# Kernel optimization log

Measured on AMD Instinct MI355X. Metric: run time of the kernel, lower is better.

## Reference

```python
import jax, jax.numpy as jnp
import numpy as np

IN_DIM, H, E_DIM = 32, 64, 16
N_NODES, N_EDGES = 50000, 100000


def setup_inputs() -> dict:
    key = jax.random.key(0)
    ks = jax.random.split(key, 12)
    x = jax.random.normal(ks[0], (N_NODES, IN_DIM), dtype=jnp.float32)
    edge_index = jax.random.randint(ks[1], (2, N_EDGES), 0, N_NODES, dtype=jnp.int64)
    edge_attr = jax.random.uniform(ks[2], (N_EDGES, E_DIM), dtype=jnp.float32)
    def lin(k, fan_in, shape):
        return jax.random.normal(k, shape, dtype=jnp.float32) / np.sqrt(fan_in)
    return {
        "x": x,
        "edge_index": edge_index,
        "edge_attr": edge_attr,
        # lin0: Linear(in_dim, h)
        "lin0_w": lin(ks[3], IN_DIM, (H, IN_DIM)),
        "lin0_b": jnp.zeros((H,), jnp.float32),
        # NNConv's edge network: Linear(edge_dim, h*h)
        "nn_w": lin(ks[4], E_DIM, (H * H, E_DIM)),
        "nn_b": jnp.zeros((H * H,), jnp.float32),
        # NNConv root weight [in_ch, out_ch] and bias
        "root": lin(ks[5], H, (H, H)),
        "conv_b": jnp.zeros((H,), jnp.float32),
        # GRU (single layer): weight_ih [3h,h], weight_hh [3h,h], biases [3h]
        "w_ih": lin(ks[6], H, (3 * H, H)),
        "w_hh": lin(ks[7], H, (3 * H, H)),
        "b_ih": jnp.zeros((3 * H,), jnp.float32),
        "b_hh": jnp.zeros((3 * H,), jnp.float32),
    }


def _nnconv(x, src, dst, edge_attr, nn_w, nn_b, root, conv_b, num_nodes):
    # per-edge weight matrices [E, h_in, h_out] from the edge MLP
    W_e = (edge_attr @ nn_w.T + nn_b).reshape(-1, H, H)
    # gather source features, per-edge matvec, scatter-add to destinations
    msg = jnp.einsum('ei,eio->eo', x[src], W_e)          # [E, h]
    agg = jax.ops.segment_sum(msg, dst, num_segments=num_nodes)
    return agg + x @ root + conv_b


def _gru_step(x, h, w_ih, w_hh, b_ih, b_hh):
    gi = x @ w_ih.T + b_ih                                # [N, 3h]
    gh = h @ w_hh.T + b_hh
    i_r, i_z, i_n = jnp.split(gi, 3, axis=-1)
    h_r, h_z, h_n = jnp.split(gh, 3, axis=-1)
    r = jax.nn.sigmoid(i_r + h_r)
    z = jax.nn.sigmoid(i_z + h_z)
    n = jnp.tanh(i_n + r * h_n)
    return (1.0 - z) * n + z * h


def reference(x, edge_index, edge_attr, lin0_w, lin0_b, nn_w, nn_b,
              root, conv_b, w_ih, w_hh, b_ih, b_hh):
    src, dst = edge_index[0], edge_index[1]
    num_nodes = x.shape[0]
    out = jax.nn.relu(x @ lin0_w.T + lin0_b)              # [N, h]
    h = out
    for _ in range(3):
        m = jax.nn.relu(_nnconv(out, src, dst, edge_attr, nn_w, nn_b,
                                root, conv_b, num_nodes))
        h = _gru_step(m, h, w_ih, w_hh, b_ih, b_hh)
        out = h
    return out
```

## Files before the change

### kernel.cpp

```cpp
#include <hip/hip_runtime.h>
#include <hip/hip_bf16.h>

typedef unsigned short u16;
typedef __attribute__((ext_vector_type(8))) _Float16 h8v;
typedef __attribute__((ext_vector_type(4))) float f32x4;

#define CAP 32

static __device__ __forceinline__ u16 f2h(float f) {
    _Float16 h = (_Float16)f;
    u16 r; __builtin_memcpy(&r, &h, 2); return r;
}
static __device__ __forceinline__ float h2f(u16 b) {
    _Float16 h; __builtin_memcpy(&h, &b, 2); return (float)h;
}
static __device__ __forceinline__ float sigm(float x) {
    return 1.f / (1.f + __expf(-x));
}
static __device__ __forceinline__ float tanh_f(float x) {
    return 1.f - 2.f / (__expf(2.f * x) + 1.f);
}

__global__ __launch_bounds__(256) void k_prep(
        const float* __restrict__ nn_w, const float* __restrict__ nn_b,
        const float* __restrict__ root, const float* __restrict__ w_hh,
        const float* __restrict__ w_ih, const float* __restrict__ lin0_w,
        const float* __restrict__ ea,
        u16* __restrict__ wf2, u16* __restrict__ w1, u16* __restrict__ w2,
        u16* __restrict__ w0, u16* __restrict__ ea16, int* __restrict__ deg,
        int N, int nEA) {
    int idx = blockIdx.x * 256 + threadIdx.x;
    if (idx < 34 * 4 * 512) {
        int j = idx & 7, lane = (idx >> 3) & 63;
        int rest = idx >> 9;
        int ct = rest & 3, kc = rest >> 2;
        int kappa = kc * 32 + ((lane >> 4) * 8) + j;
        int o = ct * 16 + (lane & 15);
        float v;
        if (kappa < 1024) {
            int k = kappa >> 6, i = kappa & 63;
            v = nn_w[(size_t)(i * 64 + o) * 16 + k];
        } else {
            v = nn_b[(size_t)(kappa - 1024) * 64 + o];
        }
        wf2[idx] = f2h(v);
    }
    if (idx < 16384 + 12288 + 2048) {
        if (idx < 16384) {
            int j = idx & 7, lane = (idx >> 3) & 63;
            int rest = idx >> 9;
            int ct = rest & 15, kc = rest >> 4;
            int k = kc * 32 + ((lane >> 4) * 8) + j;
            int col = ct * 16 + (lane & 15);
            float v = (col < 64) ? root[(size_t)k * 64 + col]
                                 : w_hh[(size_t)(col - 64) * 64 + k];
            w1[idx] = f2h(v);
        } else if (idx < 16384 + 12288) {
            int i2 = idx - 16384;
            int j = i2 & 7, lane = (i2 >> 3) & 63;
            int rest = i2 >> 9;
            int ct = rest % 12, kc = rest / 12;
            int k = kc * 32 + ((lane >> 4) * 8) + j;
            int col = ct * 16 + (lane & 15);
            w2[i2] = f2h(w_ih[(size_t)col * 64 + k]);
        } else {
            int i3 = idx - 16384 - 12288;
            int j = i3 & 7, lane = (i3 >> 3) & 63;
            int ct = i3 >> 9;
            int k = ((lane >> 4) * 8) + j;
            int col = ct * 16 + (lane & 15);
            w0[i3] = f2h(lin0_w[(size_t)col * 32 + k]);
        }
    }
    if (idx < N) deg[idx] = 0;
    if (idx < nEA) ea16[idx] = f2h(ea[idx]);
}

__global__ __launch_bounds__(256) void k_pre2(
        const int* __restrict__ ei, int* __restrict__ deg, int* __restrict__ tab,
        const float* __restrict__ x_in, const u16* __restrict__ w0,
        const float* __restrict__ lin0_b, float* __restrict__ x0,
        int N, int E) {
    int nbuild = (E + 255) / 256;
    int bid = blockIdx.x;
    int t = threadIdx.x;
    if (bid < nbuild) {
        int e = bid * 256 + t;
        if (e < E) {
            int dst = ei[E + e];
            int pos = atomicAdd(&deg[dst], 1);
            if (pos < CAP) tab[(size_t)dst * CAP + pos] = e;
        }
        return;
    }
    int b2 = bid - nbuild;
    int l = t & 63, w = t >> 6, g = l >> 4;
    int n0 = b2 * 64 + w * 16;
    int node = n0 + (l & 15);
    int nc = node < N ? node : N - 1;
    const float* xrow = x_in + (size_t)nc * 32 + g * 8;
    float4 xa = *(const float4*)(xrow);
    float4 xb = *(const float4*)(xrow + 4);
    h8v xh;
    xh[0] = (_Float16)xa.x; xh[1] = (_Float16)xa.y;
    xh[2] = (_Float16)xa.z; xh[3] = (_Float16)xa.w;
    xh[4] = (_Float16)xb.x; xh[5] = (_Float16)xb.y;
    xh[6] = (_Float16)xb.z; xh[7] = (_Float16)xb.w;
    f32x4 acc[4];
    #pragma unroll
    for (int ct = 0; ct < 4; ct++) {
        h8v wh = *(const h8v*)((const _Float16*)w0 + (ct * 64 + l) * 8);
        acc[ct] = __builtin_amdgcn_mfma_f32_16x16x32_f16(wh, xh, (f32x4)(0.f), 0, 0, 0);
    }
    if (node < N) {
        #pragma unroll
        for (int ct = 0; ct < 4; ct++) {
            int c = ct * 16 + g * 4;
            f32x4 bb = *(const f32x4*)(lin0_b + c);
            f32x4 ov;
            #pragma unroll
            for (int r = 0; r < 4; r++) ov[r] = fmaxf(acc[ct][r] + bb[r], 0.f);
            *(f32x4*)(x0 + (size_t)node * 64 + c) = ov;
        }
    }
}

__global__ __launch_bounds__(256) void k_AB(
        const float* __restrict__ x, const u16* __restrict__ ea16,
        const u16* __restrict__ wf2, const int* __restrict__ ei,
        u16* __restrict__ msg, int E) {
    __shared__ __align__(16) u16 Ab[64 * 512];
    int t = threadIdx.x, l = t & 63, w = t >> 6, g = l >> 4;
    int ctH = blockIdx.y;
    int eblk = blockIdx.x * 256 + w * 64;

    int eact[4];
    h8v xf0[4], xf1[4], eav[4][2];
    #pragma unroll
    for (int et = 0; et < 4; et++) {
        int e = eblk + et * 16 + (l & 15);
        eact[et] = e;
        int ec = e < E ? e : E - 1;
        int src = ei[ec];
        const float* xr = x + (size_t)src * 64 + g * 8;
        float4 v0 = *(const float4*)(xr);
        float4 v1 = *(const float4*)(xr + 4);
        float4 v2 = *(const float4*)(xr + 32);
        float4 v3 = *(const float4*)(xr + 36);
        h8v a, b;
        a[0] = (_Float16)v0.x; a[1] = (_Float16)v0.y;
        a[2] = (_Float16)v0.z; a[3] = (_Float16)v0.w;
        a[4] = (_Float16)v1.x; a[5] = (_Float16)v1.y;
        a[6] = (_Float16)v1.z; a[7] = (_Float16)v1.w;
        b[0] = (_Float16)v2.x; b[1] = (_Float16)v2.y;
        b[2] = (_Float16)v2.z; b[3] = (_Float16)v2.w;
        b[4] = (_Float16)v3.x; b[5] = (_Float16)v3.y;
        b[6] = (_Float16)v3.z; b[7] = (_Float16)v3.w;
        xf0[et] = a;
        xf1[et] = b;
        const _Float16* ep = (const _Float16*)ea16 + (size_t)ec * 16;
        eav[et][0] = *(const h8v*)(ep);
        eav[et][1] = *(const h8v*)(ep + 8);
    }

    const uint4* wf2u = (const uint4*)wf2;
    uint4* Abu = (uint4*)Ab;
    #pragma unroll
    for (int i = 0; i < 16; i++) {
        int j = i * 256 + t;
        int f = j >> 6, win = j & 63;
        int gf = (f >> 1) * 4 + ctH * 2 + (f & 1);
        Abu[j] = wf2u[(size_t)gf * 64 + win];
    }
    __syncthreads();

    f32x4 acc[4][2];
    #pragma unroll
    for (int et = 0; et < 4; et++)
        #pragma unroll
        for (int ct = 0; ct < 2; ct++) acc[et][ct] = (f32x4)(0.f);

    const _Float16* AbH = (const _Float16*)Ab;
    const _Float16* wfh = (const _Float16*)wf2;

    #pragma unroll
    for (int p = 0; p < 8; p++) {
        #pragma unroll
        for (int kcl = 0; kcl < 4; kcl++) {
            int kc = p * 4 + kcl;
            h8v af[2];
            #pragma unroll
            for (int ct = 0; ct < 2; ct++)
                af[ct] = *(const h8v*)(AbH + (size_t)(kc * 2 + ct) * 512 + l * 8);
            const int k = 2 * p + (kcl >> 1);
            #pragma unroll
            for (int et = 0; et < 4; et++) {
                _Float16 s = eav[et][k >> 3][k & 7];
                h8v es = {s, s, s, s, s, s, s, s};
                h8v zf = es * ((kcl & 1) ? xf1[et] : xf0[et]);
                #pragma unroll
                for (int ct = 0; ct < 2; ct++)
                    acc[et][ct] = __builtin_amdgcn_mfma_f32_16x16x32_f16(af[ct], zf, acc[et][ct], 0, 0, 0);
            }
        }
    }
    #pragma unroll
    for (int kcl = 0; kcl < 2; kcl++) {
        int kc = 32 + kcl;
        h8v af[2];
        #pragma unroll
        for (int ct = 0; ct < 2; ct++)
            af[ct] = *(const h8v*)(wfh + (size_t)(kc * 4 + ctH * 2 + ct) * 512 + l * 8);
        #pragma unroll
        for (int et = 0; et < 4; et++) {
            h8v zf = (kcl & 1) ? xf1[et] : xf0[et];
            #pragma unroll
            for (int ct = 0; ct < 2; ct++)
                acc[et][ct] = __builtin_amdgcn_mfma_f32_16x16x32_f16(af[ct], zf, acc[et][ct], 0, 0, 0);
        }
    }

    #pragma unroll
    for (int et = 0; et < 4; et++) {
        int e = eact[et];
        if (e < E) {
            u16* mr = msg + (size_t)e * 64 + g * 4;
            #pragma unroll
            for (int ct = 0; ct < 2; ct++) {
                ushort4 pk;
                pk.x = f2h(acc[et][ct][0]);
                pk.y = f2h(acc[et][ct][1]);
                pk.z = f2h(acc[et][ct][2]);
                pk.w = f2h(acc[et][ct][3]);
                *(ushort4*)(mr + (ctH * 2 + ct) * 16) = pk;
            }
        }
    }
}

__global__ __launch_bounds__(256) void k_C(
        const float* __restrict__ x, const u16* __restrict__ msg,
        const int* __restrict__ deg, const int* __restrict__ tab,
        const u16* __restrict__ w1, const u16* __restrict__ w2,
        const float* __restrict__ conv_b, const float* __restrict__ b_hh,
        const float* __restrict__ b_ih, float* __restrict__ hout, int N) {
    __shared__ float mld[4][16][68];
    int t = threadIdx.x, l = t & 63, w = t >> 6, g = l >> 4;
    int n0 = blockIdx.x * 64 + w * 16;
    int node = n0 + (l & 15);
    int nc = node < N ? node : N - 1;
    const float* xrow = x + (size_t)nc * 64 + g * 8;
    const _Float16* w1h = (const _Float16*)w1;
    const _Float16* w2h = (const _Float16*)w2;

    h8v xh[2];
    #pragma unroll
    for (int kc = 0; kc < 2; kc++) {
        f32x4 a = *(const f32x4*)(xrow + kc * 32);
        f32x4 b = *(const f32x4*)(xrow + kc * 32 + 4);
        #pragma unroll
        for (int j = 0; j < 8; j++) xh[kc][j] = (_Float16)(j < 4 ? a[j] : b[j - 4]);
    }

    f32x4 avs[4];
    #pragma unroll
    for (int ct = 0; ct < 4; ct++) avs[ct] = (f32x4)(0.f);
    if (node < N) {
        int dg = deg[node];
        dg = dg < CAP ? dg : CAP;
        const int* tr = tab + (size_t)node * CAP;
        for (int j = 0; j < dg; j++) {
            int eid = tr[j];
            const u16* mr = msg + (size_t)eid * 64 + g * 4;
            #pragma unroll
            for (int ct = 0; ct < 4; ct++) {
                ushort4 mv = *(const ushort4*)(mr + ct * 16);
                avs[ct][0] += h2f(mv.x);
                avs[ct][1] += h2f(mv.y);
                avs[ct][2] += h2f(mv.z);
                avs[ct][3] += h2f(mv.w);
            }
        }
    }

    f32x4 acc1[16];
    #pragma unroll
    for (int ct = 0; ct < 16; ct++) acc1[ct] = (f32x4)(0.f);
    #pragma unroll
    for (int kc = 0; kc < 2; kc++) {
        #pragma unroll
        for (int ct = 0; ct < 16; ct++) {
            h8v wh = *(const h8v*)(w1h + (size_t)(kc * 16 + ct) * 512 + l * 8);
            acc1[ct] = __builtin_amdgcn_mfma_f32_16x16x32_f16(wh, xh[kc], acc1[ct], 0, 0, 0);
        }
    }

    #pragma unroll
    for (int ct = 0; ct < 4; ct++) {
        int c = ct * 16 + g * 4;
        f32x4 cb = *(const f32x4*)(conv_b + c);
        f32x4 mv;
        #pragma unroll
        for (int r = 0; r < 4; r++) mv[r] = fmaxf(acc1[ct][r] + avs[ct][r] + cb[r], 0.f);
        *(f32x4*)(&mld[w][l & 15][c]) = mv;
    }
    #pragma unroll
    for (int ct = 4; ct < 16; ct++) {
        int c = (ct - 4) * 16 + g * 4;
        f32x4 bh = *(const f32x4*)(b_hh + c);
        #pragma unroll
        for (int r = 0; r < 4; r++) acc1[ct][r] += bh[r];
    }
    __syncthreads();

    h8v mh[2];
    #pragma unroll
    for (int kc = 0; kc < 2; kc++) {
        const float* mr = &mld[w][l & 15][kc * 32 + g * 8];
        f32x4 a = *(const f32x4*)(mr);
        f32x4 b = *(const f32x4*)(mr + 4);
        #pragma unroll
        for (int j = 0; j < 8; j++) mh[kc][j] = (_Float16)(j < 4 ? a[j] : b[j - 4]);
    }

    f32x4 acc2[12];
    #pragma unroll
    for (int ct = 0; ct < 12; ct++) acc2[ct] = (f32x4)(0.f);
    #pragma unroll
    for (int kc = 0; kc < 2; kc++) {
        #pragma unroll
        for (int ct = 0; ct < 12; ct++) {
            h8v wh = *(const h8v*)(w2h + (size_t)(kc * 12 + ct) * 512 + l * 8);
            acc2[ct] = __builtin_amdgcn_mfma_f32_16x16x32_f16(wh, mh[kc], acc2[ct], 0, 0, 0);
        }
    }

    #pragma unroll
    for (int q = 0; q < 4; q++) {
        int c = q * 16 + g * 4;
        f32x4 bir = *(const f32x4*)(b_ih + c);
        f32x4 biz = *(const f32x4*)(b_ih + 64 + c);
        f32x4 bin = *(const f32x4*)(b_ih + 128 + c);
        f32x4 hv = (f32x4)(0.f);
        if (node < N) hv = *(const f32x4*)(x + (size_t)node * 64 + c);
        f32x4 outv;
        #pragma unroll
        for (int r = 0; r < 4; r++) {
            float rr = sigm(acc2[q][r] + bir[r] + acc1[4 + q][r]);
            float zz = sigm(acc2[4 + q][r] + biz[r] + acc1[8 + q][r]);
            float nt = tanh_f(acc2[8 + q][r] + bin[r] + rr * acc1[12 + q][r]);
            outv[r] = (1.f - zz) * nt + zz * hv[r];
        }
        if (node < N) *(f32x4*)(hout + (size_t)node * 64 + c) = outv;
    }
}

extern "C" void kernel_launch(void* const* d_in, const int* in_sizes, int n_in,
                              void* d_out, int out_size, void* d_ws, size_t ws_size,
                              hipStream_t stream) {
    const float* x_in   = (const float*)d_in[0];
    const int*   ei     = (const int*)d_in[1];
    const float* ea     = (const float*)d_in[2];
    const float* lin0_w = (const float*)d_in[3];
    const float* lin0_b = (const float*)d_in[4];
    const float* nn_w   = (const float*)d_in[5];
    const float* nn_b   = (const float*)d_in[6];
    const float* root   = (const float*)d_in[7];
    const float* conv_b = (const float*)d_in[8];
    const float* w_ih   = (const float*)d_in[9];
    const float* w_hh   = (const float*)d_in[10];
    const float* b_ih   = (const float*)d_in[11];
    const float* b_hh   = (const float*)d_in[12];

    int N = in_sizes[0] / 32;
    int E = in_sizes[1] / 2;

    char* ws = (char*)d_ws;
    size_t off = 0;
    auto alloc = [&](size_t bytes) { char* p = ws + off; off += (bytes + 255) & ~(size_t)255; return p; };
    float* xbuf   = (float*)alloc((size_t)N * 64 * 4);
    u16*   msg    = (u16*)alloc((size_t)E * 64 * 2);
    u16*   wf2    = (u16*)alloc((size_t)34 * 4 * 512 * 2);
    u16*   ea16   = (u16*)alloc((size_t)E * 16 * 2);
    u16*   w1     = (u16*)alloc(16384 * 2);
    u16*   w2     = (u16*)alloc(12288 * 2);
    u16*   w0     = (u16*)alloc(2048 * 2);
    int*   deg    = (int*)alloc((size_t)N * 4);
    int*   tab    = (int*)alloc((size_t)N * CAP * 4);
    (void)ws_size;

    int nEA = E * 16;
    int nbuild = (E + 255) / 256;
    int ntile  = (N + 63) / 64;

    hipLaunchKernelGGL(k_prep, dim3((nEA + 255) / 256), dim3(256), 0, stream,
                       nn_w, nn_b, root, w_hh, w_ih, lin0_w, ea,
                       wf2, w1, w2, w0, ea16, deg, N, nEA);
    hipLaunchKernelGGL(k_pre2, dim3(nbuild + ntile), dim3(256), 0, stream,
                       ei, deg, tab, x_in, w0, lin0_b, xbuf, N, E);

    for (int it = 0; it < 3; it++) {
        hipLaunchKernelGGL(k_AB, dim3((E + 255) / 256, 2), dim3(256), 0, stream,
                           xbuf, ea16, wf2, ei, msg, E);
        float* hout = (it == 2) ? (float*)d_out : xbuf;
        hipLaunchKernelGGL(k_C, dim3(ntile), dim3(256), 0, stream, xbuf, msg,
                           deg, tab, w1, w2, conv_b, b_hh, b_ih, hout, N);
    }
}
```

Before: 173.6 us.

## Balance per-block edge aggregation via prefix-summed edge list and LDS atomics

Replaces the per-node serial loop over incoming messages with a block-level scheme: wave 0 prefix-sums node degrees, builds a flattened edge list in shared memory, and all 256 threads then gather 16-byte message chunks and accumulate them into a shared aggregation tile with atomicAdd. The aim is to remove load imbalance across degree-varying nodes and widen the memory accesses. In exchange it adds extra __syncthreads barriers, LDS atomic traffic, and about 17KB more shared memory per block, which may lower occupancy.

```diff
diff --git a/kernel.cpp b/kernel.cpp
--- a/kernel.cpp
+++ b/kernel.cpp
@@ -2,10 +2,12 @@
 #include <hip/hip_bf16.h>
 
 typedef unsigned short u16;
+typedef __attribute__((ext_vector_type(8))) unsigned short us8;
 typedef __attribute__((ext_vector_type(8))) _Float16 h8v;
 typedef __attribute__((ext_vector_type(4))) float f32x4;
 
 #define CAP 32
+#define ECAP 256
 
 static __device__ __forceinline__ u16 f2h(float f) {
     _Float16 h = (_Float16)f;
@@ -245,9 +247,14 @@
         const float* __restrict__ conv_b, const float* __restrict__ b_hh,
         const float* __restrict__ b_ih, float* __restrict__ hout, int N) {
     __shared__ float mld[4][16][68];
+    __shared__ float aggs[64][68];
+    __shared__ int els[ECAP];
+    __shared__ short nds[ECAP];
+    __shared__ int offs[65];
     int t = threadIdx.x, l = t & 63, w = t >> 6, g = l >> 4;
-    int n0 = blockIdx.x * 64 + w * 16;
-    int node = n0 + (l & 15);
+    int n0 = blockIdx.x * 64;
+    int nb = w * 16 + (l & 15);
+    int node = n0 + nb;
     int nc = node < N ? node : N - 1;
     const float* xrow = x + (size_t)nc * 64 + g * 8;
     const _Float16* w1h = (const _Float16*)w1;
@@ -262,26 +269,56 @@
         for (int j = 0; j < 8; j++) xh[kc][j] = (_Float16)(j < 4 ? a[j] : b[j - 4]);
     }
 
+    if (w == 0) {
+        int nd = n0 + l;
+        int d = 0;
+        if (nd < N) { d = deg[nd]; if (d > CAP) d = CAP; }
+        int s = d;
+        #pragma unroll
+        for (int o = 1; o < 64; o <<= 1) {
+            int v = __shfl_up(s, o, 64);
+            if (l >= o) s += v;
+        }
+        offs[l + 1] = s;
+        if (l == 0) offs[0] = 0;
+    }
+    {
+        float* af = &aggs[0][0];
+        for (int i = t; i < 64 * 68; i += 256) af[i] = 0.f;
+    }
+    __syncthreads();
+    int T_e = offs[64];
+
+    for (int base = 0; base < T_e; base += ECAP) {
+        int cnt = T_e - base; if (cnt > ECAP) cnt = ECAP;
+        if (w == 0) {
+            int nd = n0 + l;
+            int d = 0;
+            if (nd < N) { d = deg[nd]; if (d > CAP) d = CAP; }
+            int o = offs[l];
+            const int* tr = tab + (size_t)(nd < N ? nd : 0) * CAP;
+            for (int j = 0; j < d; j++) {
+                int s = o + j - base;
+                if (s >= 0 && s < ECAP) { els[s] = tr[j]; nds[s] = (short)l; }
+            }
+        }
+        __syncthreads();
+        for (int task = t; task < cnt * 8; task += 256) {
+            int s = task >> 3, cq = task & 7;
+            int eid = els[s];
+            int n = nds[s];
+            us8 v = *(const us8*)(msg + (size_t)eid * 64 + cq * 8);
+            #pragma unroll
+            for (int i = 0; i < 8; i++)
+                atomicAdd(&aggs[n][cq * 8 + i], h2f(v[i]));
+        }
+        __syncthreads();
+    }
+
     f32x4 avs[4];
     #pragma unroll
-    for (int ct = 0; ct < 4; ct++) avs[ct] = (f32x4)(0.f);
-    if (node < N) {
-        int dg = deg[node];
-        dg = dg < CAP ? dg : CAP;
-        const int* tr = tab + (size_t)node * CAP;
-        for (int j = 0; j < dg; j++) {
-            int eid = tr[j];
-            const u16* mr = msg + (size_t)eid * 64 + g * 4;
-            #pragma unroll
-            for (int ct = 0; ct < 4; ct++) {
-                ushort4 mv = *(const ushort4*)(mr + ct * 16);
-                avs[ct][0] += h2f(mv.x);
-                avs[ct][1] += h2f(mv.y);
-                avs[ct][2] += h2f(mv.z);
-                avs[ct][3] += h2f(mv.w);
-            }
-        }
-    }
+    for (int ct = 0; ct < 4; ct++)
+        avs[ct] = *(const f32x4*)(&aggs[nb][ct * 16 + g * 4]);
 
     f32x4 acc1[16];
     #pragma unroll
```

Result: slower. 276.3 us (+59.1%).

## Split k_C output columns across wave pairs, each wave covering two node tiles

Applied to the files above, without the earlier changes.

Previously each wave in k_C handled one 16-node tile and computed all 64 output columns, loading the full weight set per wave. Now pairs of waves share two node tiles: each wave computes half of the output column tiles for both node tiles. Each loaded weight fragment therefore feeds two MFMAs, which halves weight loads per wave and the per-wave accumulator count. The trade-off is that each wave now gathers edge messages for two nodes, each over half the channels, so per-lane gather loop iterations double while the bytes loaded per edge halve.

```diff
diff --git a/kernel.cpp b/kernel.cpp
--- a/kernel.cpp
+++ b/kernel.cpp
@@ -246,112 +246,145 @@
         const float* __restrict__ b_ih, float* __restrict__ hout, int N) {
     __shared__ float mld[4][16][68];
     int t = threadIdx.x, l = t & 63, w = t >> 6, g = l >> 4;
-    int n0 = blockIdx.x * 64 + w * 16;
-    int node = n0 + (l & 15);
-    int nc = node < N ? node : N - 1;
-    const float* xrow = x + (size_t)nc * 64 + g * 8;
+    int h = w & 1;
+    int tp = w >> 1;
+    int n0 = blockIdx.x * 64;
     const _Float16* w1h = (const _Float16*)w1;
     const _Float16* w2h = (const _Float16*)w2;
-
-    h8v xh[2];
+    int h2 = h * 2;
+
+    int tile[2], node[2];
+    h8v xh[2][2];
+    #pragma unroll
+    for (int tt = 0; tt < 2; tt++) {
+        tile[tt] = 2 * tp + tt;
+        node[tt] = n0 + tile[tt] * 16 + (l & 15);
+        int nc = node[tt] < N ? node[tt] : N - 1;
+        const float* xrow = x + (size_t)nc * 64 + g * 8;
+        #pragma unroll
+        for (int kc = 0; kc < 2; kc++) {
+            f32x4 a = *(const f32x4*)(xrow + kc * 32);
+            f32x4 b = *(const f32x4*)(xrow + kc * 32 + 4);
+            #pragma unroll
+            for (int j = 0; j < 8; j++)
+                xh[tt][kc][j] = (_Float16)(j < 4 ? a[j] : b[j - 4]);
+        }
+    }
+
+    f32x4 avs[2][2];
+    #pragma unroll
+    for (int tt = 0; tt < 2; tt++) {
+        avs[tt][0] = (f32x4)(0.f);
+        avs[tt][1] = (f32x4)(0.f);
+        if (node[tt] < N) {
+            int dg = deg[node[tt]];
+            dg = dg < CAP ? dg : CAP;
+            const int* tr = tab + (size_t)node[tt] * CAP;
+            for (int j = 0; j < dg; j++) {
+                int eid = tr[j];
+                const u16* mr = msg + (size_t)eid * 64 + g * 4;
+                #pragma unroll
+                for (int ct = 0; ct < 2; ct++) {
+                    ushort4 mv = *(const ushort4*)(mr + (h2 + ct) * 16);
+                    avs[tt][ct][0] += h2f(mv.x);
+                    avs[tt][ct][1] += h2f(mv.y);
+                    avs[tt][ct][2] += h2f(mv.z);
+                    avs[tt][ct][3] += h2f(mv.w);
+                }
+            }
+        }
+    }
+
+    f32x4 acc1[2][8];
+    #pragma unroll
+    for (int tt = 0; tt < 2; tt++)
+        #pragma unroll
+        for (int i = 0; i < 8; i++) acc1[tt][i] = (f32x4)(0.f);
     #pragma unroll
     for (int kc = 0; kc < 2; kc++) {
-        f32x4 a = *(const f32x4*)(xrow + kc * 32);
-        f32x4 b = *(const f32x4*)(xrow + kc * 32 + 4);
-        #pragma unroll
-        for (int j = 0; j < 8; j++) xh[kc][j] = (_Float16)(j < 4 ? a[j] : b[j - 4]);
-    }
-
-    f32x4 avs[4];
-    #pragma unroll
-    for (int ct = 0; ct < 4; ct++) avs[ct] = (f32x4)(0.f);
-    if (node < N) {
-        int dg = deg[node];
-        dg = dg < CAP ? dg : CAP;
-        const int* tr = tab + (size_t)node * CAP;
-        for (int j = 0; j < dg; j++) {
-            int eid = tr[j];
-            const u16* mr = msg + (size_t)eid * 64 + g * 4;
-            #pragma unroll
-            for (int ct = 0; ct < 4; ct++) {
-                ushort4 mv = *(const ushort4*)(mr + ct * 16);
-                avs[ct][0] += h2f(mv.x);
-                avs[ct][1] += h2f(mv.y);
-                avs[ct][2] += h2f(mv.z);
-                avs[ct][3] += h2f(mv.w);
+        #pragma unroll
+        for (int i = 0; i < 8; i++) {
+            int ct = (i >> 1) * 4 + h2 + (i & 1);
+            h8v wh = *(const h8v*)(w1h + (size_t)(kc * 16 + ct) * 512 + l * 8);
+            #pragma unroll
+            for (int tt = 0; tt < 2; tt++)
+                acc1[tt][i] = __builtin_amdgcn_mfma_f32_16x16x32_f16(wh, xh[tt][kc], acc1[tt][i], 0, 0, 0);
+        }
+    }
+
+    #pragma unroll
+    for (int tt = 0; tt < 2; tt++) {
+        #pragma unroll
+        for (int i = 0; i < 2; i++) {
+            int c = (h2 + i) * 16 + g * 4;
+            f32x4 cb = *(const f32x4*)(conv_b + c);
+            f32x4 mv;
+            #pragma unroll
+            for (int r = 0; r < 4; r++)
+                mv[r] = fmaxf(acc1[tt][i][r] + avs[tt][i][r] + cb[r], 0.f);
+            *(f32x4*)(&mld[tile[tt]][l & 15][c]) = mv;
+        }
+        #pragma unroll
+        for (int i = 2; i < 8; i++) {
+            int c = ((i - 2) >> 1) * 64 + (h2 + (i & 1)) * 16 + g * 4;
+            f32x4 bh = *(const f32x4*)(b_hh + c);
+            #pragma unroll
+            for (int r = 0; r < 4; r++) acc1[tt][i][r] += bh[r];
+        }
+    }
+    __syncthreads();
+
+    h8v mh[2][2];
+    #pragma unroll
+    for (int tt = 0; tt < 2; tt++) {
+        #pragma unroll
+        for (int kc = 0; kc < 2; kc++) {
+            const float* mr = &mld[tile[tt]][l & 15][kc * 32 + g * 8];
+            f32x4 a = *(const f32x4*)(mr);
+            f32x4 b = *(const f32x4*)(mr + 4);
+            #pragma unroll
+            for (int j = 0; j < 8; j++)
+                mh[tt][kc][j] = (_Float16)(j < 4 ? a[j] : b[j - 4]);
+        }
+    }
+
+    f32x4 acc2[2][6];
+    #pragma unroll
+    for (int tt = 0; tt < 2; tt++)
+        #pragma unroll
+        for (int i = 0; i < 6; i++) acc2[tt][i] = (f32x4)(0.f);
+    #pragma unroll
+    for (int kc = 0; kc < 2; kc++) {
+        #pragma unroll
+        for (int i = 0; i < 6; i++) {
+            int ct = (i >> 1) * 4 + h2 + (i & 1);
+            h8v wh = *(const h8v*)(w2h + (size_t)(kc * 12 + ct) * 512 + l * 8);
+            #pragma unroll
+            for (int tt = 0; tt < 2; tt++)
+                acc2[tt][i] = __builtin_amdgcn_mfma_f32_16x16x32_f16(wh, mh[tt][kc], acc2[tt][i], 0, 0, 0);
+        }
+    }
+
+    #pragma unroll
+    for (int tt = 0; tt < 2; tt++) {
+        #pragma unroll
+        for (int q = 0; q < 2; q++) {
+            int c = (h2 + q) * 16 + g * 4;
+            f32x4 bir = *(const f32x4*)(b_ih + c);
+            f32x4 biz = *(const f32x4*)(b_ih + 64 + c);
+            f32x4 bin = *(const f32x4*)(b_ih + 128 + c);
+            f32x4 hv = (f32x4)(0.f);
+            if (node[tt] < N) hv = *(const f32x4*)(x + (size_t)node[tt] * 64 + c);
+            f32x4 outv;
+            #pragma unroll
+            for (int r = 0; r < 4; r++) {
+                float rr = sigm(acc2[tt][q][r] + bir[r] + acc1[tt][2 + q][r]);
+                float zz = sigm(acc2[tt][2 + q][r] + biz[r] + acc1[tt][4 + q][r]);
+                float nt = tanh_f(acc2[tt][4 + q][r] + bin[r] + rr * acc1[tt][6 + q][r]);
+                outv[r] = (1.f - zz) * nt + zz * hv[r];
             }
-        }
-    }
-
-    f32x4 acc1[16];
-    #pragma unroll
-    for (int ct = 0; ct < 16; ct++) acc1[ct] = (f32x4)(0.f);
-    #pragma unroll
-    for (int kc = 0; kc < 2; kc++) {
-        #pragma unroll
-        for (int ct = 0; ct < 16; ct++) {
-            h8v wh = *(const h8v*)(w1h + (size_t)(kc * 16 + ct) * 512 + l * 8);
-            acc1[ct] = __builtin_amdgcn_mfma_f32_16x16x32_f16(wh, xh[kc], acc1[ct], 0, 0, 0);
-        }
-    }
-
-    #pragma unroll
-    for (int ct = 0; ct < 4; ct++) {
-        int c = ct * 16 + g * 4;
-        f32x4 cb = *(const f32x4*)(conv_b + c);
-        f32x4 mv;
-        #pragma unroll
-        for (int r = 0; r < 4; r++) mv[r] = fmaxf(acc1[ct][r] + avs[ct][r] + cb[r], 0.f);
-        *(f32x4*)(&mld[w][l & 15][c]) = mv;
-    }
-    #pragma unroll
-    for (int ct = 4; ct < 16; ct++) {
-        int c = (ct - 4) * 16 + g * 4;
-        f32x4 bh = *(const f32x4*)(b_hh + c);
-        #pragma unroll
-        for (int r = 0; r < 4; r++) acc1[ct][r] += bh[r];
-    }
-    __syncthreads();
-
-    h8v mh[2];
-    #pragma unroll
-    for (int kc = 0; kc < 2; kc++) {
-        const float* mr = &mld[w][l & 15][kc * 32 + g * 8];
-        f32x4 a = *(const f32x4*)(mr);
-        f32x4 b = *(const f32x4*)(mr + 4);
-        #pragma unroll
-        for (int j = 0; j < 8; j++) mh[kc][j] = (_Float16)(j < 4 ? a[j] : b[j - 4]);
-    }
-
-    f32x4 acc2[12];
-    #pragma unroll
-    for (int ct = 0; ct < 12; ct++) acc2[ct] = (f32x4)(0.f);
-    #pragma unroll
-    for (int kc = 0; kc < 2; kc++) {
-        #pragma unroll
-        for (int ct = 0; ct < 12; ct++) {
-            h8v wh = *(const h8v*)(w2h + (size_t)(kc * 12 + ct) * 512 + l * 8);
-            acc2[ct] = __builtin_amdgcn_mfma_f32_16x16x32_f16(wh, mh[kc], acc2[ct], 0, 0, 0);
-        }
-    }
-
-    #pragma unroll
-    for (int q = 0; q < 4; q++) {
-        int c = q * 16 + g * 4;
-        f32x4 bir = *(const f32x4*)(b_ih + c);
-        f32x4 biz = *(const f32x4*)(b_ih + 64 + c);
-        f32x4 bin = *(const f32x4*)(b_ih + 128 + c);
-        f32x4 hv = (f32x4)(0.f);
-        if (node < N) hv = *(const f32x4*)(x + (size_t)node * 64 + c);
-        f32x4 outv;
-        #pragma unroll
-        for (int r = 0; r < 4; r++) {
-            float rr = sigm(acc2[q][r] + bir[r] + acc1[4 + q][r]);
-            float zz = sigm(acc2[4 + q][r] + biz[r] + acc1[8 + q][r]);
-            float nt = tanh_f(acc2[8 + q][r] + bin[r] + rr * acc1[12 + q][r]);
-            outv[r] = (1.f - zz) * nt + zz * hv[r];
-        }
-        if (node < N) *(f32x4*)(hout + (size_t)node * 64 + c) = outv;
+            if (node[tt] < N) *(f32x4*)(hout + (size_t)node[tt] * 64 + c) = outv;
+        }
     }
 }
 
```

Measured after the change: 184.2 us. 6.1% more time.
